# Performance work log

Measured on AMD Instinct MI355X. Metric: run time of the kernel, lower is better.

## Reference

```python
import jax, jax.numpy as jnp
import numpy as np

B, N, DIM = 256, 196, 384
H, KD, VD = 12, 32, 32
RES = 14
EPS = 1e-5


def _build_bias_idxs():
    pts = [(i, j) for i in range(RES) for j in range(RES)]
    offs, idxs = {}, []
    for p1 in pts:
        for p2 in pts:
            o = (abs(p1[0] - p2[0]), abs(p1[1] - p2[1]))
            if o not in offs:
                offs[o] = len(offs)
            idxs.append(offs[o])
    return jnp.asarray(np.array(idxs, dtype=np.int32).reshape(N, N))


def setup_inputs() -> dict:
    key = jax.random.key(0)
    ks = jax.random.split(key, 4)
    return {
        "x": jax.random.normal(ks[0], (B, N, DIM), dtype=jnp.float32),
        "norm_w": jnp.ones((DIM,), jnp.float32),
        "norm_b": jnp.zeros((DIM,), jnp.float32),
        "qkv_w": jax.random.normal(ks[1], (H * (VD + 2 * KD), DIM), jnp.float32) * 0.02,
        "qkv_b": jnp.zeros((H * (VD + 2 * KD),), jnp.float32),
        "attention_biases": jax.random.normal(ks[2], (H, RES * RES), jnp.float32) * 0.02,
        "proj_w": jax.random.normal(ks[3], (DIM, H * VD), jnp.float32) * 0.02,
        "proj_b": jnp.zeros((DIM,), jnp.float32),
        "bias_idxs": _build_bias_idxs(),
    }


def reference(x, norm_w, norm_b, qkv_w, qkv_b, attention_biases, proj_w, proj_b, bias_idxs):
    scale = KD ** -0.5
    # LayerNorm over feature dim
    mu = jnp.mean(x, axis=-1, keepdims=True)
    var = jnp.mean(jnp.square(x - mu), axis=-1, keepdims=True)
    xn = (x - mu) * jax.lax.rsqrt(var + EPS) * norm_w + norm_b
    # QKV projection: [B,N,H*(2*KD+VD)] -> [B,N,H,*]
    qkv = (jnp.einsum("bnd,fd->bnf", xn, qkv_w) + qkv_b).reshape(B, N, H, 2 * KD + VD)
    q, k, v = qkv[..., :KD], qkv[..., KD:2 * KD], qkv[..., 2 * KD:]
    # Relative-position bias gathered into [H,N,N]
    attn_bias = attention_biases[:, bias_idxs]
    # Scores [B,H,N,N] with bias, softmax, AV
    scores = jnp.einsum("bnhk,bmhk->bhnm", q * scale, k) + attn_bias
    probs = jax.nn.softmax(scores, axis=-1)
    out = jnp.einsum("bhnm,bmhv->bnhv", probs, v).reshape(B, N, H * VD)
    return jnp.einsum("bnf,df->bnd", out, proj_w) + proj_b
```

## Files before the change

### kernel.cpp

```cpp
#include <hip/hip_runtime.h>

#define B_    256
#define N_    196
#define NP_   208
#define VSTR_ 264
#define DIM_  384
#define H_    12
#define KD_   32
#define VD_   32
#define F_    1152
#define ROWS_ (B_ * N_)
#define SCALE_ 0.17677669529663687f
#define EPS_  1e-5f

typedef __bf16 bf16_t;
typedef __bf16 bf16x2 __attribute__((ext_vector_type(2)));
typedef __bf16 bf16x4 __attribute__((ext_vector_type(4)));
typedef __bf16 bf16x8 __attribute__((ext_vector_type(8)));
typedef float  f32x4  __attribute__((ext_vector_type(4)));

__device__ __forceinline__ f32x4 mfma16(bf16x8 a, bf16x8 b, f32x4 c) {
    return __builtin_amdgcn_mfma_f32_16x16x32_bf16(a, b, c, 0, 0, 0);
}

__device__ __forceinline__ void gl2lds(const bf16_t* g, bf16_t* l) {
    __builtin_amdgcn_global_load_lds(
        (const __attribute__((address_space(1))) void*)g,
        (__attribute__((address_space(3))) void*)l, 16, 0, 0);
}

__global__ __launch_bounds__(256) void cvt_w(const float* __restrict__ src,
                                             bf16_t* __restrict__ dst) {
    const int i = (blockIdx.x * 256 + threadIdx.x) * 4;
    const float4 v = *(const float4*)(src + i);
    bf16x4 o = {(bf16_t)v.x, (bf16_t)v.y, (bf16_t)v.z, (bf16_t)v.w};
    *(bf16x4*)(dst + i) = o;
}

__global__ __launch_bounds__(256) void ln_kernel(const float* __restrict__ x,
                                                 const float* __restrict__ w,
                                                 const float* __restrict__ bvec,
                                                 bf16_t* __restrict__ xn) {
    const int lane = threadIdx.x & 63;
    const int row  = blockIdx.x * 4 + (threadIdx.x >> 6);
    const float* xr = x + (size_t)row * DIM_;
    const float4 a = *(const float4*)(xr + lane * 4);
    const float2 c = *(const float2*)(xr + 256 + lane * 2);
    float s  = a.x + a.y + a.z + a.w + c.x + c.y;
    float s2 = a.x*a.x + a.y*a.y + a.z*a.z + a.w*a.w + c.x*c.x + c.y*c.y;
    #pragma unroll
    for (int o = 32; o > 0; o >>= 1) {
        s  += __shfl_xor(s, o);
        s2 += __shfl_xor(s2, o);
    }
    const float mu = s * (1.f / 384.f);
    const float rs = rsqrtf(s2 * (1.f / 384.f) - mu * mu + EPS_);
    const float4 w4 = *(const float4*)(w + lane * 4);
    const float2 w2 = *(const float2*)(w + 256 + lane * 2);
    const float4 b4 = *(const float4*)(bvec + lane * 4);
    const float2 b2 = *(const float2*)(bvec + 256 + lane * 2);
    bf16_t* orow = xn + (size_t)row * DIM_;
    bf16x4 o4 = {(bf16_t)((a.x - mu) * rs * w4.x + b4.x),
                 (bf16_t)((a.y - mu) * rs * w4.y + b4.y),
                 (bf16_t)((a.z - mu) * rs * w4.z + b4.z),
                 (bf16_t)((a.w - mu) * rs * w4.w + b4.w)};
    *(bf16x4*)(orow + lane * 4) = o4;
    bf16x2 o2 = {(bf16_t)((c.x - mu) * rs * w2.x + b2.x),
                 (bf16_t)((c.y - mu) * rs * w2.y + b2.y)};
    *(bf16x2*)(orow + 256 + lane * 2) = o2;
}

__global__ __launch_bounds__(256) void bias_gather(const float* __restrict__ biases,
                                                   const int* __restrict__ idxs,
                                                   bf16_t* __restrict__ biasmat) {
    const int e = blockIdx.x * 256 + threadIdx.x;
    if (e >= H_ * N_ * NP_) return;
    const int h = e / (N_ * NP_);
    const int r = e % (N_ * NP_);
    const int n = r / NP_;
    const int m = r % NP_;
    const float v = (m < N_) ? biases[h * N_ + idxs[n * N_ + m]] : -1e30f;
    biasmat[e] = (bf16_t)v;
}

template <typename OutT>
__global__ __launch_bounds__(256) void gemm_mfma(const bf16_t* __restrict__ A,
                                                 const bf16_t* __restrict__ Wt,
                                                 const float* __restrict__ bias,
                                                 OutT* __restrict__ C,
                                                 int M, int Nout, int K) {
    __shared__ __align__(16) bf16_t As[128][32];
    __shared__ __align__(16) bf16_t Bs[128][32];
    const int tid  = threadIdx.x;
    const int lane = tid & 63;
    const int wv   = tid >> 6;
    const int ln   = lane & 15;
    const int ko   = lane >> 4;
    const int wr   = (wv >> 1) * 64;
    const int wc   = (wv & 1) * 64;
    const size_t bm = (size_t)blockIdx.x * 128;
    const size_t bn = (size_t)blockIdx.y * 128;

    const int srow = wv * 16 + (lane >> 2);
    const int scol = (lane & 3) * 8;
    const bf16_t* gA0 = A  + (bm + srow) * K + scol;
    const bf16_t* gA1 = gA0 + (size_t)64 * K;
    const bf16_t* gB0 = Wt + (bn + srow) * K + scol;
    const bf16_t* gB1 = gB0 + (size_t)64 * K;
    bf16_t* lA0 = &As[srow][scol];
    bf16_t* lA1 = &As[srow + 64][scol];
    bf16_t* lB0 = &Bs[srow][scol];
    bf16_t* lB1 = &Bs[srow + 64][scol];

    f32x4 acc[4][4];
    #pragma unroll
    for (int i = 0; i < 4; i++)
        #pragma unroll
        for (int j = 0; j < 4; j++)
            acc[i][j] = (f32x4){0.f, 0.f, 0.f, 0.f};

    for (int k0 = 0; k0 < K; k0 += 32) {
        gl2lds(gA0 + k0, lA0);
        gl2lds(gA1 + k0, lA1);
        gl2lds(gB0 + k0, lB0);
        gl2lds(gB1 + k0, lB1);
        __syncthreads();
        bf16x8 af[4], bfr[4];
        #pragma unroll
        for (int i = 0; i < 4; i++)
            af[i] = *(const bf16x8*)&As[wr + i * 16 + ln][ko * 8];
        #pragma unroll
        for (int j = 0; j < 4; j++)
            bfr[j] = *(const bf16x8*)&Bs[wc + j * 16 + ln][ko * 8];
        #pragma unroll
        for (int i = 0; i < 4; i++)
            #pragma unroll
            for (int j = 0; j < 4; j++)
                acc[i][j] = mfma16(af[i], bfr[j], acc[i][j]);
        __syncthreads();
    }

    #pragma unroll
    for (int j = 0; j < 4; j++) {
        const size_t col = bn + wc + j * 16 + ln;
        const float bcol = bias[col];
        #pragma unroll
        for (int i = 0; i < 4; i++)
            #pragma unroll
            for (int r = 0; r < 4; r++) {
                const size_t row = bm + wr + i * 16 + ko * 4 + r;
                C[row * Nout + col] = (OutT)(acc[i][j][r] + bcol);
            }
    }
}

__global__ __launch_bounds__(256) void attn_mfma(const bf16_t* __restrict__ qkv,
                                                 const bf16_t* __restrict__ biasmat,
                                                 bf16_t* __restrict__ out) {
    const int b = blockIdx.x / H_;
    const int h = blockIdx.x % H_;
    __shared__ __align__(16) bf16_t Ks[NP_][32];
    __shared__ __align__(16) bf16_t Vt[VD_][VSTR_];
    __shared__ __align__(16) bf16_t Pb[4][16][VSTR_];
    const int tid  = threadIdx.x;
    const int lane = tid & 63;
    const int wv   = tid >> 6;
    const int ln   = lane & 15;
    const int ko   = lane >> 4;

    {
        const int rsub = lane >> 2;
        const int col  = (lane & 3) * 8;
        for (int c = wv; c < 13; c += 4) {
            const int row = c * 16 + rsub;
            gl2lds(qkv + ((size_t)(b * N_ + row) * H_ + h) * 96 + KD_ + col,
                   &Ks[row][col]);
        }
    }
    if (tid < 224) {
        const int m  = tid;
        const int kk = (m & 15) * 16 + (m >> 4);
        const bf16_t* src = qkv + ((size_t)(b * N_ + m) * H_ + h) * 96 + 2 * KD_;
        #pragma unroll
        for (int c4 = 0; c4 < 4; c4++) {
            bf16x8 v8 = {bf16_t(0), bf16_t(0), bf16_t(0), bf16_t(0),
                         bf16_t(0), bf16_t(0), bf16_t(0), bf16_t(0)};
            if (m < N_) v8 = *(const bf16x8*)(src + c4 * 8);
            #pragma unroll
            for (int j = 0; j < 8; j++) Vt[c4 * 8 + j][kk] = v8[j];
        }
    }
    for (int e = tid; e < 32 * 32; e += 256) {
        const int v = e >> 5;
        const int s = e & 31;
        Vt[v][(s >> 1) * 16 + 14 + (s & 1)] = bf16_t(0);
    }
    __syncthreads();

    bf16x8 kf[13];
    #pragma unroll
    for (int c = 0; c < 13; c++)
        kf[c] = *(const bf16x8*)&Ks[c * 16 + ln][ko * 8];

    for (int t = wv; t < 13; t += 4) {
        const int qrow = t * 16 + ln;
        const bf16x8 qf =
            *(const bf16x8*)(qkv + ((size_t)(b * N_ + qrow) * H_ + h) * 96 + ko * 8);

        f32x4 sc[13];
        #pragma unroll
        for (int c = 0; c < 13; c++) {
            f32x4 z = {0.f, 0.f, 0.f, 0.f};
            sc[c] = mfma16(qf, kf[c], z);
        }

        float mx[4] = {-1e30f, -1e30f, -1e30f, -1e30f};
        #pragma unroll
        for (int r = 0; r < 4; r++) {
            const int rowc = min(t * 16 + ko * 4 + r, N_ - 1);
            const bf16_t* brow = biasmat + (size_t)(h * N_ + rowc) * NP_;
            #pragma unroll
            for (int c = 0; c < 13; c++) {
                const float s = sc[c][r] * SCALE_ + (float)brow[c * 16 + ln];
                sc[c][r] = s;
                mx[r] = fmaxf(mx[r], s);
            }
        }
        #pragma unroll
        for (int r = 0; r < 4; r++) {
            float m = mx[r];
            m = fmaxf(m, __shfl_xor(m, 1));
            m = fmaxf(m, __shfl_xor(m, 2));
            m = fmaxf(m, __shfl_xor(m, 4));
            m = fmaxf(m, __shfl_xor(m, 8));
            mx[r] = m;
        }
        float inv[4];
        #pragma unroll
        for (int r = 0; r < 4; r++) {
            float sum = 0.f;
            #pragma unroll
            for (int c = 0; c < 13; c++) {
                const float p = __expf(sc[c][r] - mx[r]);
                sc[c][r] = p;
                sum += p;
            }
            sum += __shfl_xor(sum, 1);
            sum += __shfl_xor(sum, 2);
            sum += __shfl_xor(sum, 4);
            sum += __shfl_xor(sum, 8);
            inv[r] = 1.f / sum;
        }
        #pragma unroll
        for (int r = 0; r < 4; r++) {
            bf16x8 pa, pb;
            #pragma unroll
            for (int c = 0; c < 8; c++) pa[c] = (bf16_t)sc[c][r];
            #pragma unroll
            for (int c = 8; c < 13; c++) pb[c - 8] = (bf16_t)sc[c][r];
            pb[5] = bf16_t(0); pb[6] = bf16_t(0); pb[7] = bf16_t(0);
            *(bf16x8*)&Pb[wv][ko * 4 + r][ln * 16]     = pa;
            *(bf16x8*)&Pb[wv][ko * 4 + r][ln * 16 + 8] = pb;
        }
        __builtin_amdgcn_s_waitcnt(0);

        f32x4 o0 = {0.f, 0.f, 0.f, 0.f};
        f32x4 o1 = {0.f, 0.f, 0.f, 0.f};
        #pragma unroll
        for (int kb = 0; kb < 8; kb++) {
            const bf16x8 pf = *(const bf16x8*)&Pb[wv][ln][kb * 32 + ko * 8];
            const bf16x8 v0 = *(const bf16x8*)&Vt[ln][kb * 32 + ko * 8];
            const bf16x8 v1 = *(const bf16x8*)&Vt[16 + ln][kb * 32 + ko * 8];
            o0 = mfma16(pf, v0, o0);
            o1 = mfma16(pf, v1, o1);
        }
        #pragma unroll
        for (int r = 0; r < 4; r++) {
            const int row = t * 16 + ko * 4 + r;
            if (row < N_) {
                const size_t ob = (size_t)(b * N_ + row) * DIM_ + h * VD_;
                out[ob + ln]      = (bf16_t)(o0[r] * inv[r]);
                out[ob + 16 + ln] = (bf16_t)(o1[r] * inv[r]);
            }
        }
    }
}

extern "C" void kernel_launch(void* const* d_in, const int* in_sizes, int n_in,
                              void* d_out, int out_size, void* d_ws, size_t ws_size,
                              hipStream_t stream) {
    const float* x        = (const float*)d_in[0];
    const float* norm_w   = (const float*)d_in[1];
    const float* norm_b   = (const float*)d_in[2];
    const float* qkv_w    = (const float*)d_in[3];
    const float* qkv_b    = (const float*)d_in[4];
    const float* att_bias = (const float*)d_in[5];
    const float* proj_w   = (const float*)d_in[6];
    const float* proj_b   = (const float*)d_in[7];
    const int*   bias_idx = (const int*)d_in[8];
    float* out = (float*)d_out;

    char* ws = (char*)d_ws;
    size_t off = 0;
    bf16_t* xn       = (bf16_t*)(ws + off); off += (size_t)ROWS_ * DIM_ * 2;
    bf16_t* qkvbuf   = (bf16_t*)(ws + off); off += (size_t)ROWS_ * F_ * 2;
    bf16_t* attn_out = (bf16_t*)(ws + off); off += (size_t)ROWS_ * DIM_ * 2;
    bf16_t* biasmat  = (bf16_t*)(ws + off); off += (size_t)H_ * N_ * NP_ * 2;
    bf16_t* wq_bf    = (bf16_t*)(ws + off); off += (size_t)F_ * DIM_ * 2;
    bf16_t* wp_bf    = (bf16_t*)(ws + off); off += (size_t)DIM_ * DIM_ * 2;

    cvt_w<<<(F_ * DIM_) / 1024, 256, 0, stream>>>(qkv_w, wq_bf);
    cvt_w<<<(DIM_ * DIM_) / 1024, 256, 0, stream>>>(proj_w, wp_bf);
    ln_kernel<<<ROWS_ / 4, 256, 0, stream>>>(x, norm_w, norm_b, xn);
    bias_gather<<<(H_ * N_ * NP_ + 255) / 256, 256, 0, stream>>>(att_bias, bias_idx, biasmat);
    gemm_mfma<bf16_t><<<dim3(ROWS_ / 128, F_ / 128), 256, 0, stream>>>(
        xn, wq_bf, qkv_b, qkvbuf, ROWS_, F_, DIM_);
    attn_mfma<<<B_ * H_, 256, 0, stream>>>(qkvbuf, biasmat, attn_out);
    gemm_mfma<float><<<dim3(ROWS_ / 128, DIM_ / 128), 256, 0, stream>>>(
        attn_out, wp_bf, proj_b, out, ROWS_, DIM_, DIM_);
}
```

Measured before the change: 377.0 us.

## Transpose MFMA operands to keep softmax probabilities in registers and vectorize stores

The attention kernel now computes scores transposed (K as the A operand), so each lane holds one query's scores. Softmax reductions need only two cross-lane shuffles, and the probabilities feed the PV MFMA straight from registers instead of going through an LDS staging buffer. To support this, the bias matrix is built transposed and padded, V is stored in a matching permuted layout, and setprio hints are added around the MFMA blocks. The GEMM also swaps operands so each lane writes four contiguous outputs as vector stores with a float4 bias load. The cost is a slightly larger bias buffer and strided bias reads in the softmax loop.

```diff
diff --git a/kernel.cpp b/kernel.cpp
--- a/kernel.cpp
+++ b/kernel.cpp
@@ -72,15 +72,15 @@
 
 __global__ __launch_bounds__(256) void bias_gather(const float* __restrict__ biases,
                                                    const int* __restrict__ idxs,
-                                                   bf16_t* __restrict__ biasmat) {
+                                                   bf16_t* __restrict__ biasT) {
     const int e = blockIdx.x * 256 + threadIdx.x;
-    if (e >= H_ * N_ * NP_) return;
-    const int h = e / (N_ * NP_);
-    const int r = e % (N_ * NP_);
-    const int n = r / NP_;
-    const int m = r % NP_;
-    const float v = (m < N_) ? biases[h * N_ + idxs[n * N_ + m]] : -1e30f;
-    biasmat[e] = (bf16_t)v;
+    if (e >= H_ * NP_ * NP_) return;
+    const int h = e / (NP_ * NP_);
+    const int r = e % (NP_ * NP_);
+    const int m = r / NP_;
+    const int q = r % NP_;
+    const float v = (m < N_ && q < N_) ? biases[h * N_ + idxs[q * N_ + m]] : -1e30f;
+    biasT[e] = (bf16_t)v;
 }
 
 template <typename OutT>
@@ -136,32 +136,40 @@
         for (int i = 0; i < 4; i++)
             #pragma unroll
             for (int j = 0; j < 4; j++)
-                acc[i][j] = mfma16(af[i], bfr[j], acc[i][j]);
+                acc[i][j] = mfma16(bfr[j], af[i], acc[i][j]);
         __syncthreads();
     }
 
     #pragma unroll
     for (int j = 0; j < 4; j++) {
-        const size_t col = bn + wc + j * 16 + ln;
-        const float bcol = bias[col];
-        #pragma unroll
-        for (int i = 0; i < 4; i++)
-            #pragma unroll
-            for (int r = 0; r < 4; r++) {
-                const size_t row = bm + wr + i * 16 + ko * 4 + r;
-                C[row * Nout + col] = (OutT)(acc[i][j][r] + bcol);
+        const int jc = wc + j * 16 + ko * 4;
+        const float4 b4 = *(const float4*)(bias + bn + jc);
+        #pragma unroll
+        for (int i = 0; i < 4; i++) {
+            const size_t row = bm + wr + i * 16 + ln;
+            const float v0 = acc[i][j][0] + b4.x;
+            const float v1 = acc[i][j][1] + b4.y;
+            const float v2 = acc[i][j][2] + b4.z;
+            const float v3 = acc[i][j][3] + b4.w;
+            OutT* dst = C + row * (size_t)Nout + bn + jc;
+            if constexpr (sizeof(OutT) == 2) {
+                bf16x4 o = {(bf16_t)v0, (bf16_t)v1, (bf16_t)v2, (bf16_t)v3};
+                *(bf16x4*)dst = o;
+            } else {
+                float4 o = {v0, v1, v2, v3};
+                *(float4*)dst = o;
             }
+        }
     }
 }
 
 __global__ __launch_bounds__(256) void attn_mfma(const bf16_t* __restrict__ qkv,
-                                                 const bf16_t* __restrict__ biasmat,
+                                                 const bf16_t* __restrict__ biasT,
                                                  bf16_t* __restrict__ out) {
     const int b = blockIdx.x / H_;
     const int h = blockIdx.x % H_;
     __shared__ __align__(16) bf16_t Ks[NP_][32];
     __shared__ __align__(16) bf16_t Vt[VD_][VSTR_];
-    __shared__ __align__(16) bf16_t Pb[4][16][VSTR_];
     const int tid  = threadIdx.x;
     const int lane = tid & 63;
     const int wv   = tid >> 6;
@@ -172,15 +180,16 @@
         const int rsub = lane >> 2;
         const int col  = (lane & 3) * 8;
         for (int c = wv; c < 13; c += 4) {
-            const int row = c * 16 + rsub;
-            gl2lds(qkv + ((size_t)(b * N_ + row) * H_ + h) * 96 + KD_ + col,
+            const int row  = c * 16 + rsub;
+            const int srow = min(row, N_ - 1);
+            gl2lds(qkv + ((size_t)(b * N_ + srow) * H_ + h) * 96 + KD_ + col,
                    &Ks[row][col]);
         }
     }
     if (tid < 224) {
         const int m  = tid;
-        const int kk = (m & 15) * 16 + (m >> 4);
-        const bf16_t* src = qkv + ((size_t)(b * N_ + m) * H_ + h) * 96 + 2 * KD_;
+        const int kk = (m & ~31) + ((m & 15) >> 2) * 8 + ((m >> 4) & 1) * 4 + (m & 3);
+        const bf16_t* src = qkv + ((size_t)(b * N_ + min(m, N_ - 1)) * H_ + h) * 96 + 2 * KD_;
         #pragma unroll
         for (int c4 = 0; c4 < 4; c4++) {
             bf16x8 v8 = {bf16_t(0), bf16_t(0), bf16_t(0), bf16_t(0),
@@ -190,11 +199,6 @@
             for (int j = 0; j < 8; j++) Vt[c4 * 8 + j][kk] = v8[j];
         }
     }
-    for (int e = tid; e < 32 * 32; e += 256) {
-        const int v = e >> 5;
-        const int s = e & 31;
-        Vt[v][(s >> 1) * 16 + 14 + (s & 1)] = bf16_t(0);
-    }
     __syncthreads();
 
     bf16x8 kf[13];
@@ -203,85 +207,75 @@
         kf[c] = *(const bf16x8*)&Ks[c * 16 + ln][ko * 8];
 
     for (int t = wv; t < 13; t += 4) {
-        const int qrow = t * 16 + ln;
+        const int q    = t * 16 + ln;
+        const int qrow = min(q, N_ - 1);
         const bf16x8 qf =
             *(const bf16x8*)(qkv + ((size_t)(b * N_ + qrow) * H_ + h) * 96 + ko * 8);
 
         f32x4 sc[13];
+        __builtin_amdgcn_s_setprio(1);
         #pragma unroll
         for (int c = 0; c < 13; c++) {
             f32x4 z = {0.f, 0.f, 0.f, 0.f};
-            sc[c] = mfma16(qf, kf[c], z);
-        }
-
-        float mx[4] = {-1e30f, -1e30f, -1e30f, -1e30f};
-        #pragma unroll
-        for (int r = 0; r < 4; r++) {
-            const int rowc = min(t * 16 + ko * 4 + r, N_ - 1);
-            const bf16_t* brow = biasmat + (size_t)(h * N_ + rowc) * NP_;
-            #pragma unroll
-            for (int c = 0; c < 13; c++) {
-                const float s = sc[c][r] * SCALE_ + (float)brow[c * 16 + ln];
+            sc[c] = mfma16(kf[c], qf, z);
+        }
+        __builtin_amdgcn_s_setprio(0);
+
+        const bf16_t* bT = biasT + ((size_t)(h * NP_) + ko * 4) * NP_ + t * 16 + ln;
+        float mx = -1e30f;
+        #pragma unroll
+        for (int c = 0; c < 13; c++)
+            #pragma unroll
+            for (int r = 0; r < 4; r++) {
+                const float s = sc[c][r] * SCALE_ + (float)bT[(c * 16 + r) * NP_];
                 sc[c][r] = s;
-                mx[r] = fmaxf(mx[r], s);
+                mx = fmaxf(mx, s);
             }
-        }
-        #pragma unroll
-        for (int r = 0; r < 4; r++) {
-            float m = mx[r];
-            m = fmaxf(m, __shfl_xor(m, 1));
-            m = fmaxf(m, __shfl_xor(m, 2));
-            m = fmaxf(m, __shfl_xor(m, 4));
-            m = fmaxf(m, __shfl_xor(m, 8));
-            mx[r] = m;
-        }
-        float inv[4];
-        #pragma unroll
-        for (int r = 0; r < 4; r++) {
-            float sum = 0.f;
-            #pragma unroll
-            for (int c = 0; c < 13; c++) {
-                const float p = __expf(sc[c][r] - mx[r]);
+        mx = fmaxf(mx, __shfl_xor(mx, 16));
+        mx = fmaxf(mx, __shfl_xor(mx, 32));
+        float sum = 0.f;
+        #pragma unroll
+        for (int c = 0; c < 13; c++)
+            #pragma unroll
+            for (int r = 0; r < 4; r++) {
+                const float p = __expf(sc[c][r] - mx);
                 sc[c][r] = p;
                 sum += p;
             }
-            sum += __shfl_xor(sum, 1);
-            sum += __shfl_xor(sum, 2);
-            sum += __shfl_xor(sum, 4);
-            sum += __shfl_xor(sum, 8);
-            inv[r] = 1.f / sum;
-        }
-        #pragma unroll
-        for (int r = 0; r < 4; r++) {
-            bf16x8 pa, pb;
-            #pragma unroll
-            for (int c = 0; c < 8; c++) pa[c] = (bf16_t)sc[c][r];
-            #pragma unroll
-            for (int c = 8; c < 13; c++) pb[c - 8] = (bf16_t)sc[c][r];
-            pb[5] = bf16_t(0); pb[6] = bf16_t(0); pb[7] = bf16_t(0);
-            *(bf16x8*)&Pb[wv][ko * 4 + r][ln * 16]     = pa;
-            *(bf16x8*)&Pb[wv][ko * 4 + r][ln * 16 + 8] = pb;
-        }
-        __builtin_amdgcn_s_waitcnt(0);
+        sum += __shfl_xor(sum, 16);
+        sum += __shfl_xor(sum, 32);
+        const float inv = 1.f / sum;
 
         f32x4 o0 = {0.f, 0.f, 0.f, 0.f};
         f32x4 o1 = {0.f, 0.f, 0.f, 0.f};
-        #pragma unroll
-        for (int kb = 0; kb < 8; kb++) {
-            const bf16x8 pf = *(const bf16x8*)&Pb[wv][ln][kb * 32 + ko * 8];
-            const bf16x8 v0 = *(const bf16x8*)&Vt[ln][kb * 32 + ko * 8];
-            const bf16x8 v1 = *(const bf16x8*)&Vt[16 + ln][kb * 32 + ko * 8];
-            o0 = mfma16(pf, v0, o0);
-            o1 = mfma16(pf, v1, o1);
-        }
-        #pragma unroll
-        for (int r = 0; r < 4; r++) {
-            const int row = t * 16 + ko * 4 + r;
-            if (row < N_) {
-                const size_t ob = (size_t)(b * N_ + row) * DIM_ + h * VD_;
-                out[ob + ln]      = (bf16_t)(o0[r] * inv[r]);
-                out[ob + 16 + ln] = (bf16_t)(o1[r] * inv[r]);
+        __builtin_amdgcn_s_setprio(1);
+        #pragma unroll
+        for (int g = 0; g < 7; g++) {
+            bf16x8 pf;
+            #pragma unroll
+            for (int jj = 0; jj < 4; jj++) pf[jj] = (bf16_t)sc[2 * g][jj];
+            if (g < 6) {
+                #pragma unroll
+                for (int jj = 0; jj < 4; jj++) pf[4 + jj] = (bf16_t)sc[2 * g + 1][jj];
+            } else {
+                pf[4] = bf16_t(0); pf[5] = bf16_t(0);
+                pf[6] = bf16_t(0); pf[7] = bf16_t(0);
             }
+            const bf16x8 v0 = *(const bf16x8*)&Vt[ln][g * 32 + ko * 8];
+            const bf16x8 v1 = *(const bf16x8*)&Vt[16 + ln][g * 32 + ko * 8];
+            o0 = mfma16(v0, pf, o0);
+            o1 = mfma16(v1, pf, o1);
+        }
+        __builtin_amdgcn_s_setprio(0);
+
+        if (q < N_) {
+            bf16_t* dst = out + (size_t)(b * N_ + q) * DIM_ + h * VD_ + ko * 4;
+            bf16x4 oa = {(bf16_t)(o0[0] * inv), (bf16_t)(o0[1] * inv),
+                         (bf16_t)(o0[2] * inv), (bf16_t)(o0[3] * inv)};
+            bf16x4 ob = {(bf16_t)(o1[0] * inv), (bf16_t)(o1[1] * inv),
+                         (bf16_t)(o1[2] * inv), (bf16_t)(o1[3] * inv)};
+            *(bf16x4*)dst = oa;
+            *(bf16x4*)(dst + 16) = ob;
         }
     }
 }
@@ -305,17 +299,17 @@
     bf16_t* xn       = (bf16_t*)(ws + off); off += (size_t)ROWS_ * DIM_ * 2;
     bf16_t* qkvbuf   = (bf16_t*)(ws + off); off += (size_t)ROWS_ * F_ * 2;
     bf16_t* attn_out = (bf16_t*)(ws + off); off += (size_t)ROWS_ * DIM_ * 2;
-    bf16_t* biasmat  = (bf16_t*)(ws + off); off += (size_t)H_ * N_ * NP_ * 2;
+    bf16_t* biasT    = (bf16_t*)(ws + off); off += (size_t)H_ * NP_ * NP_ * 2;
     bf16_t* wq_bf    = (bf16_t*)(ws + off); off += (size_t)F_ * DIM_ * 2;
     bf16_t* wp_bf    = (bf16_t*)(ws + off); off += (size_t)DIM_ * DIM_ * 2;
 
     cvt_w<<<(F_ * DIM_) / 1024, 256, 0, stream>>>(qkv_w, wq_bf);
     cvt_w<<<(DIM_ * DIM_) / 1024, 256, 0, stream>>>(proj_w, wp_bf);
     ln_kernel<<<ROWS_ / 4, 256, 0, stream>>>(x, norm_w, norm_b, xn);
-    bias_gather<<<(H_ * N_ * NP_ + 255) / 256, 256, 0, stream>>>(att_bias, bias_idx, biasmat);
+    bias_gather<<<(H_ * NP_ * NP_ + 255) / 256, 256, 0, stream>>>(att_bias, bias_idx, biasT);
     gemm_mfma<bf16_t><<<dim3(ROWS_ / 128, F_ / 128), 256, 0, stream>>>(
         xn, wq_bf, qkv_b, qkvbuf, ROWS_, F_, DIM_);
-    attn_mfma<<<B_ * H_, 256, 0, stream>>>(qkvbuf, biasmat, attn_out);
+    attn_mfma<<<B_ * H_, 256, 0, stream>>>(qkvbuf, biasT, attn_out);
     gemm_mfma<float><<<dim3(ROWS_ / 128, DIM_ / 128), 256, 0, stream>>>(
         attn_out, wp_bf, proj_b, out, ROWS_, DIM_, DIM_);
 }
```

Result: faster. 358.6 us, median of 2 (-4.9%).
